# Kernel optimization log

Measured on AMD Instinct MI355X. Metric: run time of the kernel, lower is better.

## Reference

```python
import jax, jax.numpy as jnp
import numpy as np

N_STREAMS = 4
TAU = 1.0
ALPHA = 0.1
CAYLEY_ITERS = 2
LN_EPS = 1e-5


def setup_inputs() -> dict:
    key = jax.random.key(0)
    k1, k2, k3 = jax.random.split(key, 3)
    b, l, d = 2, 4096, 2048
    n = N_STREAMS
    x = jax.random.normal(k1, (b, l, d), dtype=jnp.float32)
    ln_w = jnp.ones((d,), dtype=jnp.float32)
    ln_b = jnp.zeros((d,), dtype=jnp.float32)
    # CastedLinear: trunc_normal std = 1/sqrt(in_features)
    proj_w = jax.random.truncated_normal(k2, -2.0, 2.0, (3 * n * n, d), dtype=jnp.float32) / jnp.sqrt(d * 1.0)
    proj_b = jnp.zeros((3 * n * n,), dtype=jnp.float32)
    # sublayer_fn realized as a dense linear (typical transformer sublayer core)
    W_sub = jax.random.normal(k3, (d, d), dtype=jnp.float32) / jnp.sqrt(d * 1.0)
    return {"x": x, "ln_w": ln_w, "ln_b": ln_b, "proj_w": proj_w, "proj_b": proj_b, "W_sub": W_sub}


def _layernorm(x, w, b):
    mu = jnp.mean(x, axis=-1, keepdims=True)
    var = jnp.mean(jnp.square(x - mu), axis=-1, keepdims=True)
    return (x - mu) * jax.lax.rsqrt(var + LN_EPS) * w + b


def _iterative_cayley(raw):
    # raw: (b, l, n, n) fp32
    w = raw - jnp.swapaxes(raw, -1, -2)
    eye = jnp.eye(N_STREAMS, dtype=raw.dtype)
    y = eye + ALPHA * w
    for _ in range(CAYLEY_ITERS):
        y = eye + 0.5 * ALPHA * jnp.matmul(w, eye + y)
    return y


def reference(x, ln_w, ln_b, proj_w, proj_b, W_sub):
    b, l, d = x.shape
    n = N_STREAMS
    gates = _layernorm(x, ln_w, ln_b) @ proj_w.T + proj_b  # (b, l, 3*n*n)
    pre_raw, post_raw, res_raw = jnp.split(gates, 3, axis=-1)
    pre_raw = pre_raw.reshape(b, l, n, n).astype(jnp.float32)
    post_raw = post_raw.reshape(b, l, n, n).astype(jnp.float32)
    res_raw = res_raw.reshape(b, l, n, n).astype(jnp.float32)
    h_pre = jax.nn.softmax(pre_raw / TAU, axis=-1)
    h_post = jax.nn.softmax(post_raw / TAU, axis=-2)
    h_res = _iterative_cayley(res_raw)
    # All streams of x_streams are identical copies of x, so
    # einsum('blij,bljd->blid', h, x_streams).mean(-2) == mean_i(sum_j h[i,j]) * x.
    coeff_pre = jnp.mean(jnp.sum(h_pre, axis=-1), axis=-1)    # (b, l)
    coeff_res = jnp.mean(jnp.sum(h_res, axis=-1), axis=-1)    # (b, l)
    coeff_post = jnp.mean(jnp.sum(h_post, axis=-1), axis=-1)  # (b, l)
    x_in = coeff_pre[..., None] * x
    y = x_in @ W_sub  # sublayer_fn
    return coeff_res[..., None] * x + coeff_post[..., None] * y
```

## Files before the change

kernel.cpp:

```cpp
#include <hip/hip_runtime.h>
#include <stdint.h>


typedef __attribute__((ext_vector_type(8))) __bf16 bf16x8;
typedef __attribute__((ext_vector_type(4))) float f32x4;
typedef __attribute__((ext_vector_type(8))) unsigned short us8;
typedef __attribute__((ext_vector_type(4))) unsigned short us4;

__device__ __forceinline__ unsigned short f2bf(float f) {
  union { float f; unsigned int u; } v; v.f = f;
  unsigned int u = v.u;
  u += 0x7fffu + ((u >> 16) & 1u);
  return (unsigned short)(u >> 16);
}

__device__ __forceinline__ float bf2f(unsigned short u) {
  union { unsigned int u; float f; } v; v.u = (unsigned int)u << 16;
  return v.f;
}

__device__ __forceinline__ void gload_lds16(const void* g, void* l) {
  __builtin_amdgcn_global_load_lds(
      (__attribute__((address_space(1))) void*)g,
      (__attribute__((address_space(3))) void*)l, 16, 0, 0);
}

__global__ __launch_bounds__(256) void k_lnx(
    const float* __restrict__ x, unsigned short* __restrict__ xb,
    float2* __restrict__ mur, int D) {
  const int t = blockIdx.x;
  const int tid = threadIdx.x;
  const float* row = x + (size_t)t * D;
  f32x4 a = *(const f32x4*)(row + tid * 8);
  f32x4 b = *(const f32x4*)(row + tid * 8 + 4);
  float vv[8] = {a[0], a[1], a[2], a[3], b[0], b[1], b[2], b[3]};
  float s = 0.f, ss = 0.f;
#pragma unroll
  for (int j = 0; j < 8; ++j) { s += vv[j]; ss += vv[j] * vv[j]; }
#pragma unroll
  for (int off = 32; off > 0; off >>= 1) { s += __shfl_down(s, off); ss += __shfl_down(ss, off); }
  __shared__ float red[8];
  int lane = tid & 63, wv = tid >> 6;
  if (lane == 0) { red[wv] = s; red[4 + wv] = ss; }
  __syncthreads();
  if (tid == 0) {
    float S = red[0] + red[1] + red[2] + red[3];
    float SS = red[4] + red[5] + red[6] + red[7];
    float mu = S / (float)D;
    float var = SS / (float)D - mu * mu;
    float2 o; o.x = mu; o.y = rsqrtf(var + 1e-5f);
    mur[t] = o;
  }
  us8 ox;
#pragma unroll
  for (int j = 0; j < 8; ++j) ox[j] = f2bf(vv[j]);
  *(us8*)(xb + (size_t)t * D + tid * 8) = ox;
}

__global__ __launch_bounds__(256) void k_wt(const float* __restrict__ W,
                                            unsigned short* __restrict__ Wt, int D) {
  __shared__ float tile[64][65];
  int kb = blockIdx.x * 64, nb = blockIdx.y * 64;
  int tid = threadIdx.x;
  int tx = tid & 15, ty = tid >> 4;
#pragma unroll
  for (int p = 0; p < 4; ++p) {
    int r = p * 16 + ty;
    f32x4 v = *(const f32x4*)(W + (size_t)(kb + r) * D + nb + tx * 4);
    tile[r][tx * 4 + 0] = v[0]; tile[r][tx * 4 + 1] = v[1];
    tile[r][tx * 4 + 2] = v[2]; tile[r][tx * 4 + 3] = v[3];
  }
  __syncthreads();
#pragma unroll
  for (int p = 0; p < 2; ++p) {
    int c = p * 256 + tid;
    int nr = c >> 3, kc = (c & 7) * 8;
    us8 o;
#pragma unroll
    for (int j = 0; j < 8; ++j) o[j] = f2bf(tile[kc + j][nr]);
    *(us8*)(Wt + (size_t)(nb + nr) * D + kb + kc) = o;
  }
}

__global__ __launch_bounds__(256) void k_wp(
    const float* __restrict__ P, const float* __restrict__ w, const float* __restrict__ b,
    unsigned short* __restrict__ WPb, float* __restrict__ S, float* __restrict__ T, int K) {
  const int j = blockIdx.x, tid = threadIdx.x;
  float s = 0.f, t = 0.f;
  for (int i = tid * 4; i < K; i += 1024) {
    f32x4 pv = *(const f32x4*)(P + (size_t)j * K + i);
    f32x4 wv = *(const f32x4*)(w + i);
    f32x4 bv = *(const f32x4*)(b + i);
    us4 o;
#pragma unroll
    for (int q = 0; q < 4; ++q) {
      float wp = pv[q] * wv[q];
      o[q] = f2bf(wp);
      s += wp;
      t += pv[q] * bv[q];
    }
    *(us4*)(WPb + (size_t)j * K + i) = o;
  }
#pragma unroll
  for (int off = 32; off > 0; off >>= 1) { s += __shfl_down(s, off); t += __shfl_down(t, off); }
  __shared__ float rs[4], rt[4];
  int lane = tid & 63, wvi = tid >> 6;
  if (lane == 0) { rs[wvi] = s; rt[wvi] = t; }
  __syncthreads();
  if (tid == 0) {
    S[j] = rs[0] + rs[1] + rs[2] + rs[3];
    T[j] = rt[0] + rt[1] + rt[2] + rt[3];
  }
}

__global__ __launch_bounds__(256) void k_gates(
    const unsigned short* __restrict__ A,
    const unsigned short* __restrict__ Bp,
    const float* __restrict__ pb,
    const float2* __restrict__ mur,
    const float* __restrict__ S, const float* __restrict__ T,
    float* __restrict__ cresp, float* __restrict__ cpyp, int K) {
  __shared__ __attribute__((aligned(16))) unsigned short As[128 * 32];
  __shared__ __attribute__((aligned(16))) unsigned short Bs[48 * 32];
  __shared__ float gl[128][49];
  __shared__ float pbs[48], Ss[48], Ts[48];
  int tid = threadIdx.x, lane = tid & 63, wv = tid >> 6;
  if (tid < 48) { pbs[tid] = pb[tid]; Ss[tid] = S[tid]; Ts[tid] = T[tid]; }
  f32x4 acc[2][3] = {};
  size_t rowBase = (size_t)blockIdx.x * 128;
  for (int k0 = 0; k0 < K; k0 += 32) {
#pragma unroll
    for (int inst = 0; inst < 2; ++inst) {
      int eo = inst * 2048 + wv * 512 + lane * 8;
      int r = eo >> 5, cc = eo & 31;
      gload_lds16(A + (rowBase + r) * K + k0 + cc, (char*)As + inst * 4096 + wv * 1024);
    }
    if (tid < 192) {
      int r = tid >> 2, cc = (tid & 3) * 8;
      us8 v = *(const us8*)(Bp + (size_t)r * K + k0 + cc);
      *(us8*)(Bs + r * 32 + cc) = v;
    }
    __syncthreads();
    int kb = (lane >> 4) * 8, rr = lane & 15;
    bf16x8 av[2], bv[3];
#pragma unroll
    for (int mi = 0; mi < 2; ++mi)
      av[mi] = *(const bf16x8*)(As + (wv * 32 + mi * 16 + rr) * 32 + kb);
#pragma unroll
    for (int ni = 0; ni < 3; ++ni)
      bv[ni] = *(const bf16x8*)(Bs + (ni * 16 + rr) * 32 + kb);
#pragma unroll
    for (int mi = 0; mi < 2; ++mi)
#pragma unroll
      for (int ni = 0; ni < 3; ++ni)
        acc[mi][ni] = __builtin_amdgcn_mfma_f32_16x16x32_bf16(av[mi], bv[ni], acc[mi][ni], 0, 0, 0);
    __syncthreads();
  }
#pragma unroll
  for (int mi = 0; mi < 2; ++mi)
#pragma unroll
    for (int ni = 0; ni < 3; ++ni)
#pragma unroll
      for (int i = 0; i < 4; ++i)
        gl[wv * 32 + mi * 16 + (lane >> 4) * 4 + i][ni * 16 + (lane & 15)] = acc[mi][ni][i];
  __syncthreads();
  if (tid < 128) {
    float2 mr = mur[rowBase + tid];
    const float rmu = mr.y * mr.x;
    float g[48];
#pragma unroll
    for (int j = 0; j < 48; ++j) g[j] = mr.y * gl[tid][j] - rmu * Ss[j] + Ts[j] + pbs[j];
    float cpre = 0.f;
#pragma unroll
    for (int i = 0; i < 4; ++i) {
      float m = fmaxf(fmaxf(g[i * 4], g[i * 4 + 1]), fmaxf(g[i * 4 + 2], g[i * 4 + 3]));
      float e0 = expf(g[i * 4] - m), e1 = expf(g[i * 4 + 1] - m);
      float e2 = expf(g[i * 4 + 2] - m), e3 = expf(g[i * 4 + 3] - m);
      float inv = 1.f / (e0 + e1 + e2 + e3);
      cpre += e0 * inv + e1 * inv + e2 * inv + e3 * inv;
    }
    cpre *= 0.25f;
    float cpost = 0.f;
#pragma unroll
    for (int j = 0; j < 4; ++j) {
      float a0 = g[16 + j], a1 = g[20 + j], a2 = g[24 + j], a3 = g[28 + j];
      float m = fmaxf(fmaxf(a0, a1), fmaxf(a2, a3));
      float e0 = expf(a0 - m), e1 = expf(a1 - m), e2 = expf(a2 - m), e3 = expf(a3 - m);
      float inv = 1.f / (e0 + e1 + e2 + e3);
      cpost += e0 * inv + e1 * inv + e2 * inv + e3 * inv;
    }
    cpost *= 0.25f;
    float w4[16], y4[16];
#pragma unroll
    for (int i = 0; i < 4; ++i)
#pragma unroll
      for (int j = 0; j < 4; ++j)
        w4[i * 4 + j] = g[32 + i * 4 + j] - g[32 + j * 4 + i];
#pragma unroll
    for (int i = 0; i < 16; ++i) y4[i] = 0.1f * w4[i];
    y4[0] += 1.f; y4[5] += 1.f; y4[10] += 1.f; y4[15] += 1.f;
#pragma unroll
    for (int it = 0; it < 2; ++it) {
      float z[16];
#pragma unroll
      for (int i = 0; i < 16; ++i) z[i] = y4[i];
      z[0] += 1.f; z[5] += 1.f; z[10] += 1.f; z[15] += 1.f;
#pragma unroll
      for (int i = 0; i < 4; ++i)
#pragma unroll
        for (int j = 0; j < 4; ++j) {
          float acc2 = 0.f;
#pragma unroll
          for (int k = 0; k < 4; ++k) acc2 += w4[i * 4 + k] * z[k * 4 + j];
          y4[i * 4 + j] = ((i == j) ? 1.f : 0.f) + 0.05f * acc2;
        }
    }
    float cr = 0.f;
#pragma unroll
    for (int i = 0; i < 16; ++i) cr += y4[i];
    cr *= 0.25f;
    cresp[rowBase + tid] = cr;
    cpyp[rowBase + tid] = cpre * cpost;
  }
}

__global__ __launch_bounds__(512, 2) void k_gemm(
    const unsigned short* __restrict__ A,
    const unsigned short* __restrict__ Bt,
    const unsigned short* __restrict__ xbr,
    const float* __restrict__ cresp, const float* __restrict__ cpyp,
    float* __restrict__ out, int M, int N, int K) {
  __shared__ __attribute__((aligned(16))) unsigned short As[4][256 * 32];
  __shared__ __attribute__((aligned(16))) unsigned short Bs[4][256 * 32];
  const int tid = threadIdx.x, lane = tid & 63, wv = tid >> 6;
  const int nbm = M >> 8;
  const int nwg = nbm * (N >> 8);
  const int chunk = nwg >> 3;
  const int gid = (blockIdx.x & 7) * chunk + (blockIdx.x >> 3);
  const int bn = gid / nbm, bm = gid % nbm;
  const int wm = wv >> 2, wn = wv & 3;
  const int rr = lane & 15, ksl = lane >> 4;
  const int koff = (ksl ^ ((rr >> 1) & 3)) * 8;
  const int rloc = tid >> 2;
  const int cbelem = ((tid & 3) ^ ((tid >> 3) & 3)) * 8;
  const unsigned short* aG = A + (size_t)((bm << 8) + rloc) * K + cbelem;
  const unsigned short* bG = Bt + (size_t)((bn << 8) + rloc) * K + cbelem;
  f32x4 acc[8][4] = {};
  const int nsl = K >> 5;

#define STAGE(KT, SLOT)                                                        \
  {                                                                            \
    const unsigned short* ag_ = aG + (KT) * 32;                                \
    const unsigned short* bg_ = bG + (KT) * 32;                                \
    unsigned short* la_ = &As[(SLOT)][wv * 512];                               \
    unsigned short* lb_ = &Bs[(SLOT)][wv * 512];                               \
    gload_lds16(ag_, la_);                                                     \
    gload_lds16(ag_ + (size_t)128 * K, la_ + 4096);                            \
    gload_lds16(bg_, lb_);                                                     \
    gload_lds16(bg_ + (size_t)128 * K, lb_ + 4096);                            \
  }

  STAGE(0, 0)
  STAGE(1, 1)
  STAGE(2, 2)

#define GBODY(S)                                                               \
  {                                                                            \
    asm volatile("s_waitcnt vmcnt(8)" ::: "memory");                           \
    __builtin_amdgcn_sched_barrier(0);                                         \
    __builtin_amdgcn_s_barrier();                                              \
    __builtin_amdgcn_sched_barrier(0);                                         \
    int kt_ = jb + (S) + 3;                                                    \
    if (kt_ > nsl - 1) kt_ = nsl - 1;                                          \
    STAGE(kt_, ((S) + 3) & 3)                                                  \
    __builtin_amdgcn_sched_barrier(0);                                         \
    const unsigned short* Ab = &As[(S)][(wm * 128 + rr) * 32 + koff];          \
    const unsigned short* Bb = &Bs[(S)][(wn * 64 + rr) * 32 + koff];           \
    bf16x8 av[8], bv[4];                                                       \
    _Pragma("unroll")                                                          \
    for (int mf = 0; mf < 8; ++mf) av[mf] = *(const bf16x8*)(Ab + mf * 512);   \
    _Pragma("unroll")                                                          \
    for (int nf = 0; nf < 4; ++nf) bv[nf] = *(const bf16x8*)(Bb + nf * 512);   \
    __builtin_amdgcn_s_setprio(1);                                             \
    _Pragma("unroll")                                                          \
    for (int mf = 0; mf < 8; ++mf)                                             \
      _Pragma("unroll")                                                        \
      for (int nf = 0; nf < 4; ++nf)                                           \
        acc[mf][nf] =                                                          \
            __builtin_amdgcn_mfma_f32_16x16x32_bf16(av[mf], bv[nf],            \
                                                    acc[mf][nf], 0, 0, 0);     \
    __builtin_amdgcn_s_setprio(0);                                             \
  }

  for (int jb = 0; jb < nsl; jb += 4) {
    GBODY(0)
    GBODY(1)
    GBODY(2)
    GBODY(3)
  }
#undef GBODY
#undef STAGE

  const int orow0 = (bm << 8) + wm * 128 + ksl * 4;
  const int ocol0 = (bn << 8) + wn * 64 + rr;
#pragma unroll
  for (int mf = 0; mf < 8; ++mf)
#pragma unroll
    for (int i = 0; i < 4; ++i) {
      const int row = orow0 + mf * 16 + i;
      const float crv = cresp[row], cpv = cpyp[row];
      const size_t base = (size_t)row * N + ocol0;
#pragma unroll
      for (int nf = 0; nf < 4; ++nf)
        out[base + nf * 16] = crv * bf2f(xbr[base + nf * 16]) + cpv * acc[mf][nf][i];
    }
}

extern "C" void kernel_launch(void* const* d_in, const int* in_sizes, int n_in,
                              void* d_out, int out_size, void* d_ws, size_t ws_size,
                              hipStream_t stream) {
  const float* x  = (const float*)d_in[0];
  const float* lw = (const float*)d_in[1];
  const float* lb = (const float*)d_in[2];
  const float* pw = (const float*)d_in[3];
  const float* pb = (const float*)d_in[4];
  const float* W  = (const float*)d_in[5];
  float* out = (float*)d_out;

  const int D = in_sizes[1];
  const int M = in_sizes[0] / D;
  const int G = in_sizes[4];

  char* ws = (char*)d_ws;
  size_t off = 0;
  unsigned short* xb  = (unsigned short*)(ws + off); off += (size_t)M * D * 2;
  unsigned short* Wt  = (unsigned short*)(ws + off); off += (size_t)D * D * 2;
  unsigned short* WPb = (unsigned short*)(ws + off); off += (size_t)G * D * 2;
  float2* mur = (float2*)(ws + off); off += (size_t)M * 8;
  float* Sv   = (float*)(ws + off); off += 64 * 4;
  float* Tv   = (float*)(ws + off); off += 64 * 4;
  float* cres = (float*)(ws + off); off += (size_t)M * 4;
  float* cpy  = (float*)(ws + off); off += (size_t)M * 4;

  k_lnx<<<M, 256, 0, stream>>>(x, xb, mur, D);
  k_wt<<<dim3(D / 64, D / 64), 256, 0, stream>>>(W, Wt, D);
  k_wp<<<G, 256, 0, stream>>>(pw, lw, lb, WPb, Sv, Tv, D);
  k_gates<<<M / 128, 256, 0, stream>>>(xb, WPb, pb, mur, Sv, Tv, cres, cpy, D);

  const int nwg = (M / 256) * (D / 256);
  k_gemm<<<nwg, 512, 0, stream>>>(xb, Wt, xb, cres, cpy, out, M, D, D);
}
```

Baseline: 133.2 us.

## Fuse layernorm stats and bf16 cast into gates GEMM, merge weight prep kernels

Merges the W transpose/cast kernel and the proj weight prep kernel into one launch that splits work by block index. Folds the per-row layernorm statistics and the bf16 conversion of x into the gates kernel, which now streams fp32 x directly, computes mean/rstd on the fly, writes xb, and feeds the MFMA gate projection with 32-row tiles. This removes two launches and one pass over x plus the intermediate mean/rstd buffer. In exchange, the gates kernel uses smaller tiles with only two of four waves doing MFMA, and each slice is bracketed by two barriers.

```diff
diff --git a/kernel.cpp b/kernel.cpp
--- a/kernel.cpp
+++ b/kernel.cpp
@@ -25,151 +25,139 @@
       (__attribute__((address_space(3))) void*)l, 16, 0, 0);
 }
 
-__global__ __launch_bounds__(256) void k_lnx(
-    const float* __restrict__ x, unsigned short* __restrict__ xb,
-    float2* __restrict__ mur, int D) {
-  const int t = blockIdx.x;
+__global__ __launch_bounds__(256) void k_wtp(
+    const float* __restrict__ W, unsigned short* __restrict__ Wt,
+    const float* __restrict__ P, const float* __restrict__ w, const float* __restrict__ b,
+    unsigned short* __restrict__ WPb, float* __restrict__ S, float* __restrict__ T, int D) {
+  __shared__ float tile[64][65];
+  __shared__ float rs[4], rt[4];
   const int tid = threadIdx.x;
-  const float* row = x + (size_t)t * D;
-  f32x4 a = *(const f32x4*)(row + tid * 8);
-  f32x4 b = *(const f32x4*)(row + tid * 8 + 4);
-  float vv[8] = {a[0], a[1], a[2], a[3], b[0], b[1], b[2], b[3]};
+  const int nwt = (D >> 6) * (D >> 6);
+  if ((int)blockIdx.x < nwt) {
+    const int bx = blockIdx.x;
+    const int kb = (bx & ((D >> 6) - 1)) * 64, nb = (bx / (D >> 6)) * 64;
+    const int tx = tid & 15, ty = tid >> 4;
+#pragma unroll
+    for (int p = 0; p < 4; ++p) {
+      int r = p * 16 + ty;
+      f32x4 v = *(const f32x4*)(W + (size_t)(kb + r) * D + nb + tx * 4);
+      tile[r][tx * 4 + 0] = v[0]; tile[r][tx * 4 + 1] = v[1];
+      tile[r][tx * 4 + 2] = v[2]; tile[r][tx * 4 + 3] = v[3];
+    }
+    __syncthreads();
+#pragma unroll
+    for (int p = 0; p < 2; ++p) {
+      int c = p * 256 + tid;
+      int nr = c >> 3, kc = (c & 7) * 8;
+      us8 o;
+#pragma unroll
+      for (int j = 0; j < 8; ++j) o[j] = f2bf(tile[kc + j][nr]);
+      *(us8*)(Wt + (size_t)(nb + nr) * D + kb + kc) = o;
+    }
+  } else {
+    const int j = blockIdx.x - nwt;
+    float s = 0.f, t = 0.f;
+    for (int i = tid * 4; i < D; i += 1024) {
+      f32x4 pv = *(const f32x4*)(P + (size_t)j * D + i);
+      f32x4 wv = *(const f32x4*)(w + i);
+      f32x4 bv = *(const f32x4*)(b + i);
+      us4 o;
+#pragma unroll
+      for (int q = 0; q < 4; ++q) {
+        float wp = pv[q] * wv[q];
+        o[q] = f2bf(wp);
+        s += wp;
+        t += pv[q] * bv[q];
+      }
+      *(us4*)(WPb + (size_t)j * D + i) = o;
+    }
+#pragma unroll
+    for (int off = 32; off > 0; off >>= 1) { s += __shfl_down(s, off); t += __shfl_down(t, off); }
+    const int lane = tid & 63, wvi = tid >> 6;
+    if (lane == 0) { rs[wvi] = s; rt[wvi] = t; }
+    __syncthreads();
+    if (tid == 0) {
+      S[j] = rs[0] + rs[1] + rs[2] + rs[3];
+      T[j] = rt[0] + rt[1] + rt[2] + rt[3];
+    }
+  }
+}
+
+__global__ __launch_bounds__(256) void k_lngates(
+    const float* __restrict__ x,
+    const unsigned short* __restrict__ WPb,
+    const float* __restrict__ pb,
+    const float* __restrict__ S, const float* __restrict__ T,
+    unsigned short* __restrict__ xb,
+    float* __restrict__ cresp, float* __restrict__ cpyp, int K) {
+  __shared__ __attribute__((aligned(16))) unsigned short As[32 * 40];
+  __shared__ __attribute__((aligned(16))) unsigned short Bs[48 * 40];
+  __shared__ float gl[32][49];
+  __shared__ float pbs[48], Ss[48], Ts[48];
+  __shared__ float smu[32], srd[32];
+  const int tid = threadIdx.x, lane = tid & 63, wv = tid >> 6;
+  const size_t rowBase = (size_t)blockIdx.x * 32;
+  if (tid < 48) { pbs[tid] = pb[tid]; Ss[tid] = S[tid]; Ts[tid] = T[tid]; }
+  const int arow = tid >> 3, ac8 = tid & 7;
+  const float* gx = x + (rowBase + arow) * (size_t)K + ac8 * 4;
+  unsigned short* gxb = xb + (rowBase + arow) * (size_t)K + ac8 * 4;
+  const int br = tid >> 2, bc = (tid & 3) * 8;
+  const unsigned short* gB = WPb + (size_t)br * K + bc;
+  f32x4 acc[3] = {};
   float s = 0.f, ss = 0.f;
-#pragma unroll
-  for (int j = 0; j < 8; ++j) { s += vv[j]; ss += vv[j] * vv[j]; }
-#pragma unroll
-  for (int off = 32; off > 0; off >>= 1) { s += __shfl_down(s, off); ss += __shfl_down(ss, off); }
-  __shared__ float red[8];
-  int lane = tid & 63, wv = tid >> 6;
-  if (lane == 0) { red[wv] = s; red[4 + wv] = ss; }
+  const int nsl = K >> 5;
+  f32x4 xn = *(const f32x4*)gx;
+  us8 bn = {};
+  if (tid < 192) bn = *(const us8*)gB;
+  for (int sl = 0; sl < nsl; ++sl) {
+    f32x4 xc = xn;
+    us8 bcur = bn;
+    if (sl + 1 < nsl) {
+      xn = *(const f32x4*)(gx + (sl + 1) * 32);
+      if (tid < 192) bn = *(const us8*)(gB + (sl + 1) * 32);
+    }
+    __syncthreads();
+    us4 ox;
+#pragma unroll
+    for (int q = 0; q < 4; ++q) { float v = xc[q]; s += v; ss += v * v; ox[q] = f2bf(v); }
+    *(us4*)(As + arow * 40 + ac8 * 4) = ox;
+    *(us4*)(gxb + sl * 32) = ox;
+    if (tid < 192) *(us8*)(Bs + br * 40 + bc) = bcur;
+    __syncthreads();
+    if (wv < 2) {
+      const int rr = lane & 15, cc2 = (lane >> 4) * 8;
+      bf16x8 av = *(const bf16x8*)(As + (wv * 16 + rr) * 40 + cc2);
+#pragma unroll
+      for (int ni = 0; ni < 3; ++ni) {
+        bf16x8 bvf = *(const bf16x8*)(Bs + (ni * 16 + rr) * 40 + cc2);
+        acc[ni] = __builtin_amdgcn_mfma_f32_16x16x32_bf16(av, bvf, acc[ni], 0, 0, 0);
+      }
+    }
+  }
+  if (wv < 2) {
+#pragma unroll
+    for (int ni = 0; ni < 3; ++ni)
+#pragma unroll
+      for (int i = 0; i < 4; ++i)
+        gl[wv * 16 + (lane >> 4) * 4 + i][ni * 16 + (lane & 15)] = acc[ni][i];
+  }
+#pragma unroll
+  for (int off = 4; off > 0; off >>= 1) {
+    s += __shfl_down(s, off, 8);
+    ss += __shfl_down(ss, off, 8);
+  }
+  if ((tid & 7) == 0) {
+    float mu = s / (float)K;
+    float var = ss / (float)K - mu * mu;
+    smu[arow] = mu;
+    srd[arow] = rsqrtf(var + 1e-5f);
+  }
   __syncthreads();
-  if (tid == 0) {
-    float S = red[0] + red[1] + red[2] + red[3];
-    float SS = red[4] + red[5] + red[6] + red[7];
-    float mu = S / (float)D;
-    float var = SS / (float)D - mu * mu;
-    float2 o; o.x = mu; o.y = rsqrtf(var + 1e-5f);
-    mur[t] = o;
-  }
-  us8 ox;
-#pragma unroll
-  for (int j = 0; j < 8; ++j) ox[j] = f2bf(vv[j]);
-  *(us8*)(xb + (size_t)t * D + tid * 8) = ox;
-}
-
-__global__ __launch_bounds__(256) void k_wt(const float* __restrict__ W,
-                                            unsigned short* __restrict__ Wt, int D) {
-  __shared__ float tile[64][65];
-  int kb = blockIdx.x * 64, nb = blockIdx.y * 64;
-  int tid = threadIdx.x;
-  int tx = tid & 15, ty = tid >> 4;
-#pragma unroll
-  for (int p = 0; p < 4; ++p) {
-    int r = p * 16 + ty;
-    f32x4 v = *(const f32x4*)(W + (size_t)(kb + r) * D + nb + tx * 4);
-    tile[r][tx * 4 + 0] = v[0]; tile[r][tx * 4 + 1] = v[1];
-    tile[r][tx * 4 + 2] = v[2]; tile[r][tx * 4 + 3] = v[3];
-  }
-  __syncthreads();
-#pragma unroll
-  for (int p = 0; p < 2; ++p) {
-    int c = p * 256 + tid;
-    int nr = c >> 3, kc = (c & 7) * 8;
-    us8 o;
-#pragma unroll
-    for (int j = 0; j < 8; ++j) o[j] = f2bf(tile[kc + j][nr]);
-    *(us8*)(Wt + (size_t)(nb + nr) * D + kb + kc) = o;
-  }
-}
-
-__global__ __launch_bounds__(256) void k_wp(
-    const float* __restrict__ P, const float* __restrict__ w, const float* __restrict__ b,
-    unsigned short* __restrict__ WPb, float* __restrict__ S, float* __restrict__ T, int K) {
-  const int j = blockIdx.x, tid = threadIdx.x;
-  float s = 0.f, t = 0.f;
-  for (int i = tid * 4; i < K; i += 1024) {
-    f32x4 pv = *(const f32x4*)(P + (size_t)j * K + i);
-    f32x4 wv = *(const f32x4*)(w + i);
-    f32x4 bv = *(const f32x4*)(b + i);
-    us4 o;
-#pragma unroll
-    for (int q = 0; q < 4; ++q) {
-      float wp = pv[q] * wv[q];
-      o[q] = f2bf(wp);
-      s += wp;
-      t += pv[q] * bv[q];
-    }
-    *(us4*)(WPb + (size_t)j * K + i) = o;
-  }
-#pragma unroll
-  for (int off = 32; off > 0; off >>= 1) { s += __shfl_down(s, off); t += __shfl_down(t, off); }
-  __shared__ float rs[4], rt[4];
-  int lane = tid & 63, wvi = tid >> 6;
-  if (lane == 0) { rs[wvi] = s; rt[wvi] = t; }
-  __syncthreads();
-  if (tid == 0) {
-    S[j] = rs[0] + rs[1] + rs[2] + rs[3];
-    T[j] = rt[0] + rt[1] + rt[2] + rt[3];
-  }
-}
-
-__global__ __launch_bounds__(256) void k_gates(
-    const unsigned short* __restrict__ A,
-    const unsigned short* __restrict__ Bp,
-    const float* __restrict__ pb,
-    const float2* __restrict__ mur,
-    const float* __restrict__ S, const float* __restrict__ T,
-    float* __restrict__ cresp, float* __restrict__ cpyp, int K) {
-  __shared__ __attribute__((aligned(16))) unsigned short As[128 * 32];
-  __shared__ __attribute__((aligned(16))) unsigned short Bs[48 * 32];
-  __shared__ float gl[128][49];
-  __shared__ float pbs[48], Ss[48], Ts[48];
-  int tid = threadIdx.x, lane = tid & 63, wv = tid >> 6;
-  if (tid < 48) { pbs[tid] = pb[tid]; Ss[tid] = S[tid]; Ts[tid] = T[tid]; }
-  f32x4 acc[2][3] = {};
-  size_t rowBase = (size_t)blockIdx.x * 128;
-  for (int k0 = 0; k0 < K; k0 += 32) {
-#pragma unroll
-    for (int inst = 0; inst < 2; ++inst) {
-      int eo = inst * 2048 + wv * 512 + lane * 8;
-      int r = eo >> 5, cc = eo & 31;
-      gload_lds16(A + (rowBase + r) * K + k0 + cc, (char*)As + inst * 4096 + wv * 1024);
-    }
-    if (tid < 192) {
-      int r = tid >> 2, cc = (tid & 3) * 8;
-      us8 v = *(const us8*)(Bp + (size_t)r * K + k0 + cc);
-      *(us8*)(Bs + r * 32 + cc) = v;
-    }
-    __syncthreads();
-    int kb = (lane >> 4) * 8, rr = lane & 15;
-    bf16x8 av[2], bv[3];
-#pragma unroll
-    for (int mi = 0; mi < 2; ++mi)
-      av[mi] = *(const bf16x8*)(As + (wv * 32 + mi * 16 + rr) * 32 + kb);
-#pragma unroll
-    for (int ni = 0; ni < 3; ++ni)
-      bv[ni] = *(const bf16x8*)(Bs + (ni * 16 + rr) * 32 + kb);
-#pragma unroll
-    for (int mi = 0; mi < 2; ++mi)
-#pragma unroll
-      for (int ni = 0; ni < 3; ++ni)
-        acc[mi][ni] = __builtin_amdgcn_mfma_f32_16x16x32_bf16(av[mi], bv[ni], acc[mi][ni], 0, 0, 0);
-    __syncthreads();
-  }
-#pragma unroll
-  for (int mi = 0; mi < 2; ++mi)
-#pragma unroll
-    for (int ni = 0; ni < 3; ++ni)
-#pragma unroll
-      for (int i = 0; i < 4; ++i)
-        gl[wv * 32 + mi * 16 + (lane >> 4) * 4 + i][ni * 16 + (lane & 15)] = acc[mi][ni][i];
-  __syncthreads();
-  if (tid < 128) {
-    float2 mr = mur[rowBase + tid];
-    const float rmu = mr.y * mr.x;
+  if (tid < 32) {
+    const float mu = smu[tid], r = srd[tid], rmu = r * mu;
     float g[48];
 #pragma unroll
-    for (int j = 0; j < 48; ++j) g[j] = mr.y * gl[tid][j] - rmu * Ss[j] + Ts[j] + pbs[j];
+    for (int j = 0; j < 48; ++j) g[j] = r * gl[tid][j] - rmu * Ss[j] + Ts[j] + pbs[j];
     float cpre = 0.f;
 #pragma unroll
     for (int i = 0; i < 4; ++i) {
@@ -336,16 +324,14 @@
   unsigned short* xb  = (unsigned short*)(ws + off); off += (size_t)M * D * 2;
   unsigned short* Wt  = (unsigned short*)(ws + off); off += (size_t)D * D * 2;
   unsigned short* WPb = (unsigned short*)(ws + off); off += (size_t)G * D * 2;
-  float2* mur = (float2*)(ws + off); off += (size_t)M * 8;
   float* Sv   = (float*)(ws + off); off += 64 * 4;
   float* Tv   = (float*)(ws + off); off += 64 * 4;
   float* cres = (float*)(ws + off); off += (size_t)M * 4;
   float* cpy  = (float*)(ws + off); off += (size_t)M * 4;
 
-  k_lnx<<<M, 256, 0, stream>>>(x, xb, mur, D);
-  k_wt<<<dim3(D / 64, D / 64), 256, 0, stream>>>(W, Wt, D);
-  k_wp<<<G, 256, 0, stream>>>(pw, lw, lb, WPb, Sv, Tv, D);
-  k_gates<<<M / 128, 256, 0, stream>>>(xb, WPb, pb, mur, Sv, Tv, cres, cpy, D);
+  const int nwt = (D / 64) * (D / 64);
+  k_wtp<<<nwt + G, 256, 0, stream>>>(W, Wt, pw, lw, lb, WPb, Sv, Tv, D);
+  k_lngates<<<M / 32, 256, 0, stream>>>(x, WPb, pb, Sv, Tv, xb, cres, cpy, D);
 
   const int nwg = (M / 256) * (D / 256);
   k_gemm<<<nwg, 512, 0, stream>>>(xb, Wt, xb, cres, cpy, out, M, D, D);
```

After: 116.8 us (median of 2 runs). 1.14x faster.
